# Kernel optimization log

Measured on AMD Instinct MI355X. Metric: run time of the kernel, lower is better.

Reference implementation:

```python
import jax, jax.numpy as jnp
import numpy as np

DOWNSAMPLE = 4
REG = 0.05
SINKHORN_ITERS = 50
LAMBDA_OT = 1.0
LAMBDA_TV = 1.0


def setup_inputs() -> dict:
    key = jax.random.key(0)
    k1, k2 = jax.random.split(key)
    pred = jax.random.uniform(k1, (16, 1, 256, 256), dtype=jnp.float32)
    gt = jax.random.uniform(k2, (16, 1, 256, 256), dtype=jnp.float32)
    return {"pred": pred, "gt": gt, "epoch": 5, "max_epoch": 10}


def _avg_pool(x, k):
    B, C, H, W = x.shape
    return x.reshape(B, C, H // k, k, W // k, k).mean(axis=(3, 5))


def _normalize(x, n):
    # relu then normalize to a distribution; fall back to uniform if sum==0
    x = jnp.maximum(x, 0.0)
    s = x.sum(axis=1, keepdims=True)  # [B,1]
    return jnp.where(s > 0, x / s, jnp.full_like(x, 1.0 / n))


def _curriculum_loss(pred, gt, epoch, max_epoch):
    B = pred.shape[0]
    # --- counting loss: L1 between total counts ---
    pc = pred.reshape(B, -1).sum(axis=1)
    gc = gt.reshape(B, -1).sum(axis=1)
    l_count = jnp.abs(pc - gc).mean()

    t = float(epoch) / float(max(1, max_epoch))
    ot_w = LAMBDA_OT * t
    tv_w = LAMBDA_TV * t

    # --- OT loss (batched Sinkhorn) ---
    pd = _avg_pool(pred, DOWNSAMPLE)
    gd = _avg_pool(gt, DOWNSAMPLE)
    h, w = pd.shape[2], pd.shape[3]
    n = h * w
    ys = jnp.arange(h, dtype=jnp.float32)
    xs = jnp.arange(w, dtype=jnp.float32)
    yy, xx = jnp.meshgrid(ys, xs, indexing="ij")
    yf = yy.reshape(-1)  # [n]
    xf = xx.reshape(-1)
    # squared euclidean cost matrix [n,n], built separably (no [n,n,2] temp)
    M = (yf[:, None] - yf[None, :]) ** 2 + (xf[:, None] - xf[None, :]) ** 2
    K = jnp.exp(-M / REG)  # [n,n]

    a = _normalize(pd.reshape(B, -1), n)  # [B,n]
    b = _normalize(gd.reshape(B, -1), n)

    def step(uv, _):
        u, v = uv
        u = a / (v @ K.T)  # K @ v per sample, batched
        v = b / (u @ K)    # K.T @ u per sample, batched
        return (u, v), None

    ones = jnp.ones((B, n), dtype=pred.dtype)
    (u, v), _ = jax.lax.scan(step, (ones, ones), None, length=SINKHORN_ITERS)
    # cost_b = sum_ij u_i K_ij v_j M_ij
    cost = jnp.einsum("bn,nm,bm->b", u, K * M, v)
    l_ot = cost.mean()

    # --- total variation loss ---
    dx = jnp.abs(pred[:, :, :, 1:] - pred[:, :, :, :-1]).mean()
    dy = jnp.abs(pred[:, :, 1:, :] - pred[:, :, :-1, :]).mean()
    l_tv = dx + dy

    return l_count + ot_w * l_ot + tv_w * l_tv


def reference(pred, gt, epoch, max_epoch):
    return _curriculum_loss(pred, gt, epoch, max_epoch)
```

## Files before the change

kernel.cpp:

```cpp
#include <hip/hip_runtime.h>
#include <math.h>


#define KW1 2.0611536224385578e-09f
#define MW2 8.4967085105831778e-18f
#define RP2 72
#define PDOFF 2048
#define GDOFF 67584

__device__ __forceinline__ float dpp_left(float x) {
  return __int_as_float(__builtin_amdgcn_update_dpp(
      0, __float_as_int(x), 0x111, 0xF, 0xF, true));
}
__device__ __forceinline__ float dpp_right(float x) {
  return __int_as_float(__builtin_amdgcn_update_dpp(
      0, __float_as_int(x), 0x101, 0xF, 0xF, true));
}

__device__ __forceinline__ float ad4(const float4 a, const float4 b) {
  return fabsf(a.x - b.x) + fabsf(a.y - b.y) + fabsf(a.z - b.z) + fabsf(a.w - b.w);
}

__device__ __forceinline__ float agent_ld(const float* p) {
  return __hip_atomic_load(p, __ATOMIC_RELAXED, __HIP_MEMORY_SCOPE_AGENT);
}

__device__ __forceinline__ void hrow4(const float f[4], float h[4]) {
  const float l = dpp_left(f[3]);
  const float r = dpp_right(f[0]);
  h[0] = fmaf(KW1, l + f[1], f[0]);
  h[1] = fmaf(KW1, f[0] + f[2], f[1]);
  h[2] = fmaf(KW1, f[1] + f[3], f[2]);
  h[3] = fmaf(KW1, f[2] + r, f[3]);
}

__device__ __forceinline__ void phase_core(
    const float prev[4][4], float ph[4][4],
    const float cf0[4], const float cf3[4],
    float2 mA, float4 mB, float2 mC, float2 pA, float4 pB, float2 pC,
    float* __restrict__ RT_wr, float* __restrict__ RB_wr, int wb,
    float out0[4], float out3[4]) {
  hrow4(prev[0], ph[0]); hrow4(prev[1], ph[1]);
  hrow4(prev[2], ph[2]); hrow4(prev[3], ph[3]);
  float hm[4], hp[4];
  hm[0] = fmaf(KW1, mA.y + mB.y, mB.x);
  hm[1] = fmaf(KW1, mB.x + mB.z, mB.y);
  hm[2] = fmaf(KW1, mB.y + mB.w, mB.z);
  hm[3] = fmaf(KW1, mB.z + mC.x, mB.w);
  hp[0] = fmaf(KW1, pA.y + pB.y, pB.x);
  hp[1] = fmaf(KW1, pB.x + pB.z, pB.y);
  hp[2] = fmaf(KW1, pB.y + pB.w, pB.z);
  hp[3] = fmaf(KW1, pB.z + pC.x, pB.w);
#pragma unroll
  for (int j = 0; j < 4; ++j)
    out0[j] = cf0[j] * __builtin_amdgcn_rcpf(fmaf(KW1, hm[j] + ph[1][j], ph[0][j]));
#pragma unroll
  for (int j = 0; j < 4; ++j)
    out3[j] = cf3[j] * __builtin_amdgcn_rcpf(fmaf(KW1, ph[2][j] + hp[j], ph[3][j]));
  *(float4*)&RT_wr[wb] = make_float4(out0[0], out0[1], out0[2], out0[3]);
  *(float4*)&RB_wr[wb] = make_float4(out3[0], out3[1], out3[2], out3[3]);
}

__global__ __launch_bounds__(256) void prep_kernel(
    const float* __restrict__ pred, const float* __restrict__ gt,
    float* __restrict__ ws) {
  __shared__ float rbuf[16];
  const int g = blockIdx.x;
  const int im = g >> 4, band = g & 15;
  const int t = threadIdx.x;
  const int ppy = t >> 6, ppx = t & 63;
  const float* pb = pred + im * 65536;
  const float* gb = gt + im * 65536;
  const int sr0 = band * 16 + ppy * 4;
  const int c0 = ppx * 4;

  float4 q[4];
  float ps = 0.f, gs = 0.f, sx = 0.f, sy = 0.f;
#pragma unroll
  for (int r = 0; r < 4; ++r) {
    q[r] = *(const float4*)(pb + (sr0 + r) * 256 + c0);
    const float4 e = *(const float4*)(gb + (sr0 + r) * 256 + c0);
    ps += (q[r].x + q[r].y) + (q[r].z + q[r].w);
    gs += (e.x + e.y) + (e.z + e.w);
    sx += fabsf(q[r].y - q[r].x) + fabsf(q[r].z - q[r].y) + fabsf(q[r].w - q[r].z);
    const float nf = __shfl_down(q[r].x, 1);
    if (ppx < 63) sx += fabsf(nf - q[r].w);
  }
  sy += ad4(q[1], q[0]) + ad4(q[2], q[1]) + ad4(q[3], q[2]);
  if (sr0 + 4 < 256) {
    const float4 qn = *(const float4*)(pb + (sr0 + 4) * 256 + c0);
    sy += ad4(qn, q[3]);
  }
  const int prow = band * 4 + ppy;
  ws[PDOFF + im * 4096 + prow * 64 + ppx] = fmaxf(ps * 0.0625f, 0.f);
  ws[GDOFF + im * 4096 + prow * 64 + ppx] = fmaxf(gs * 0.0625f, 0.f);

  float r0 = ps, r1 = gs, r2 = sx, r3 = sy;
#pragma unroll
  for (int o = 32; o > 0; o >>= 1) {
    r0 += __shfl_down(r0, o); r1 += __shfl_down(r1, o);
    r2 += __shfl_down(r2, o); r3 += __shfl_down(r3, o);
  }
  if ((t & 63) == 0) {
    const int w = t >> 6;
    rbuf[w * 4 + 0] = r0; rbuf[w * 4 + 1] = r1;
    rbuf[w * 4 + 2] = r2; rbuf[w * 4 + 3] = r3;
  }
  __syncthreads();
  if (t == 0) {
    float a0 = 0, a1 = 0, a2 = 0, a3 = 0;
    for (int w = 0; w < 4; ++w) {
      a0 += rbuf[w * 4]; a1 += rbuf[w * 4 + 1];
      a2 += rbuf[w * 4 + 2]; a3 += rbuf[w * 4 + 3];
    }
    ws[g] = a0; ws[256 + g] = a1; ws[512 + g] = a2; ws[768 + g] = a3;
  }
}

__global__ __launch_bounds__(256) void sink_kernel(
    float* __restrict__ ws, const int* __restrict__ epoch,
    const int* __restrict__ max_epoch, float* __restrict__ out,
    unsigned int* __restrict__ cnt) {
  __shared__ float RTu[18 * RP2], RBu[18 * RP2];
  __shared__ float RTv[18 * RP2], RBv[18 * RP2];
  __shared__ float rbuf[24];
  __shared__ int lastflag;

  const int b = blockIdx.x;
  const int t = threadIdx.x;
  const int tyg = t >> 4, tx = t & 15;
  const int y0 = tyg * 4, x0 = tx * 4;

  for (int i = t; i < 18 * RP2; i += 256) {
    RTu[i] = 0.f; RBu[i] = 0.f; RTv[i] = 0.f; RBv[i] = 0.f;
  }

  float pdv[4][4], gdv[4][4];
  float spd = 0.f, sgd = 0.f;
#pragma unroll
  for (int i = 0; i < 4; ++i) {
    const float4 qa = *(const float4*)&ws[PDOFF + b * 4096 + (y0 + i) * 64 + x0];
    pdv[i][0] = qa.x; pdv[i][1] = qa.y; pdv[i][2] = qa.z; pdv[i][3] = qa.w;
    spd += (qa.x + qa.y) + (qa.z + qa.w);
    const float4 qb = *(const float4*)&ws[GDOFF + b * 4096 + (y0 + i) * 64 + x0];
    gdv[i][0] = qb.x; gdv[i][1] = qb.y; gdv[i][2] = qb.z; gdv[i][3] = qb.w;
    sgd += (qb.x + qb.y) + (qb.z + qb.w);
  }
  float r2 = spd, r3 = sgd;
#pragma unroll
  for (int o = 32; o > 0; o >>= 1) { r2 += __shfl_down(r2, o); r3 += __shfl_down(r3, o); }
  if ((t & 63) == 0) { rbuf[(t >> 6) * 2] = r2; rbuf[(t >> 6) * 2 + 1] = r3; }
  __syncthreads();
  if (t == 0) {
    rbuf[16] = rbuf[0] + rbuf[2] + rbuf[4] + rbuf[6];
    rbuf[17] = rbuf[1] + rbuf[3] + rbuf[5] + rbuf[7];
  }
  __syncthreads();
  const float Sp = rbuf[16], Sg = rbuf[17];

  float av[4][4], bv[4][4];
#pragma unroll
  for (int i = 0; i < 4; ++i)
#pragma unroll
    for (int j = 0; j < 4; ++j) {
      av[i][j] = (Sp > 0.f) ? (pdv[i][j] / Sp) : (1.f / 4096.f);
      bv[i][j] = (Sg > 0.f) ? (gdv[i][j] / Sg) : (1.f / 4096.f);
    }

  const int rbb = tyg * RP2 + x0 + 2;
  const int rtb = (tyg + 2) * RP2 + x0 + 2;
  const int wb  = (1 + tyg) * RP2 + 4 + x0;

  float uu[4][4], vv[4][4], uh[4][4], vh[4][4];
#pragma unroll
  for (int i = 0; i < 4; ++i)
#pragma unroll
    for (int j = 0; j < 4; ++j) vv[i][j] = 1.f;
  *(float4*)&RTv[wb] = make_float4(1.f, 1.f, 1.f, 1.f);
  *(float4*)&RBv[wb] = make_float4(1.f, 1.f, 1.f, 1.f);
  __syncthreads();

#pragma unroll 1
  for (int it = 0; it < 50; ++it) {
    {
      const float2 mA = *(const float2*)&RBv[rbb];
      const float4 mB = *(const float4*)&RBv[rbb + 2];
      const float2 mC = *(const float2*)&RBv[rbb + 6];
      const float2 pA = *(const float2*)&RTv[rtb];
      const float4 pB = *(const float4*)&RTv[rtb + 2];
      const float2 pC = *(const float2*)&RTv[rtb + 6];
      if (it != 0) {
#pragma unroll
        for (int j = 0; j < 4; ++j) {
          vv[1][j] = bv[1][j] * __builtin_amdgcn_rcpf(fmaf(KW1, uh[0][j] + uh[2][j], uh[1][j]));
          vv[2][j] = bv[2][j] * __builtin_amdgcn_rcpf(fmaf(KW1, uh[1][j] + uh[3][j], uh[2][j]));
        }
      }
      phase_core(vv, vh, av[0], av[3], mA, mB, mC, pA, pB, pC,
                 RTu, RBu, wb, uu[0], uu[3]);
    }
    __syncthreads();
    {
      const float2 mA = *(const float2*)&RBu[rbb];
      const float4 mB = *(const float4*)&RBu[rbb + 2];
      const float2 mC = *(const float2*)&RBu[rbb + 6];
      const float2 pA = *(const float2*)&RTu[rtb];
      const float4 pB = *(const float4*)&RTu[rtb + 2];
      const float2 pC = *(const float2*)&RTu[rtb + 6];
#pragma unroll
      for (int j = 0; j < 4; ++j) {
        uu[1][j] = av[1][j] * __builtin_amdgcn_rcpf(fmaf(KW1, vh[0][j] + vh[2][j], vh[1][j]));
        uu[2][j] = av[2][j] * __builtin_amdgcn_rcpf(fmaf(KW1, vh[1][j] + vh[3][j], vh[2][j]));
      }
      phase_core(uu, uh, bv[0], bv[3], mA, mB, mC, pA, pB, pC,
                 RTv, RBv, wb, vv[0], vv[3]);
    }
    __syncthreads();
  }
#pragma unroll
  for (int j = 0; j < 4; ++j) {
    vv[1][j] = bv[1][j] * __builtin_amdgcn_rcpf(fmaf(KW1, uh[0][j] + uh[2][j], uh[1][j]));
    vv[2][j] = bv[2][j] * __builtin_amdgcn_rcpf(fmaf(KW1, uh[1][j] + uh[3][j], uh[2][j]));
  }

  float c = 0.f;
  {
    const float2 mA = *(const float2*)&RBv[rbb];
    const float4 mB = *(const float4*)&RBv[rbb + 2];
    const float2 mC = *(const float2*)&RBv[rbb + 6];
    const float2 pA = *(const float2*)&RTv[rtb];
    const float4 pB = *(const float4*)&RTv[rtb + 2];
    const float2 pC = *(const float2*)&RTv[rtb + 6];
    float W[6][6];
    W[0][0] = mA.y; W[0][1] = mB.x; W[0][2] = mB.y;
    W[0][3] = mB.z; W[0][4] = mB.w; W[0][5] = mC.x;
    W[5][0] = pA.y; W[5][1] = pB.x; W[5][2] = pB.y;
    W[5][3] = pB.z; W[5][4] = pB.w; W[5][5] = pC.x;
#pragma unroll
    for (int i = 0; i < 4; ++i) {
      W[1 + i][0] = dpp_left(vv[i][3]);
      W[1 + i][5] = dpp_right(vv[i][0]);
#pragma unroll
      for (int j = 0; j < 4; ++j) W[1 + i][1 + j] = vv[i][j];
    }
#pragma unroll
    for (int i = 0; i < 4; ++i)
#pragma unroll
      for (int j = 0; j < 4; ++j) {
        const float e = (W[i][j + 1] + W[i + 2][j + 1])
                      + (W[i + 1][j] + W[i + 1][j + 2]);
        const float d = (W[i][j] + W[i][j + 2])
                      + (W[i + 2][j] + W[i + 2][j + 2]);
        c += uu[i][j] * fmaf(MW2, d, KW1 * e);
      }
  }
#pragma unroll
  for (int o = 32; o > 0; o >>= 1) c += __shfl_down(c, o);
  if ((t & 63) == 0) rbuf[t >> 6] = c;
  __syncthreads();
  if (t == 0) {
    ws[1024 + b] = rbuf[0] + rbuf[1] + rbuf[2] + rbuf[3];
    __threadfence();
    const unsigned int old = atomicAdd(cnt, 1u);
    lastflag = (old == 15u) ? 1 : 0;
  }
  __syncthreads();

  if (lastflag) {
    __threadfence();
    float myPc = agent_ld(&ws[t]);
    float myGc = agent_ld(&ws[256 + t]);
    float myTx = agent_ld(&ws[512 + t]);
    float myTy = agent_ld(&ws[768 + t]);
#pragma unroll
    for (int o = 8; o > 0; o >>= 1) {
      myPc += __shfl_down(myPc, o, 16);
      myGc += __shfl_down(myGc, o, 16);
    }
    float d = ((t & 15) == 0) ? fabsf(myPc - myGc) : 0.f;
    float ct = (t < 16) ? agent_ld(&ws[1024 + t]) : 0.f;
#pragma unroll
    for (int o = 32; o > 0; o >>= 1) {
      d += __shfl_down(d, o); ct += __shfl_down(ct, o);
      myTx += __shfl_down(myTx, o); myTy += __shfl_down(myTy, o);
    }
    if ((t & 63) == 0) {
      const int w = t >> 6;
      rbuf[w * 4] = d; rbuf[w * 4 + 1] = ct;
      rbuf[w * 4 + 2] = myTx; rbuf[w * 4 + 3] = myTy;
    }
    __syncthreads();
    if (t == 0) {
      float lc = 0, lot = 0, tvx = 0, tvy = 0;
      for (int w = 0; w < 4; ++w) {
        lc += rbuf[w * 4]; lot += rbuf[w * 4 + 1];
        tvx += rbuf[w * 4 + 2]; tvy += rbuf[w * 4 + 3];
      }
      int me = max_epoch[0]; if (me < 1) me = 1;
      const float tt = (float)epoch[0] / (float)me;
      const float ltv = tvx / (16.f * 256.f * 255.f) + tvy / (16.f * 255.f * 256.f);
      out[0] = lc * (1.f / 16.f) + tt * (lot * (1.f / 16.f)) + tt * ltv;
    }
  }
}

__global__ __launch_bounds__(256) void fused_fallback(
    const float* __restrict__ pred, const float* __restrict__ gt,
    float* __restrict__ ws, const int* __restrict__ epoch,
    const int* __restrict__ max_epoch, float* __restrict__ out,
    unsigned int* __restrict__ cnt) {
  __shared__ float RTu[18 * RP2], RBu[18 * RP2];
  __shared__ float RTv[18 * RP2], RBv[18 * RP2];
  __shared__ float rbuf[24];

  const int b = blockIdx.x;
  const int t = threadIdx.x;
  const int tyg = t >> 4, tx = t & 15;
  const int y0 = tyg * 4, x0 = tx * 4;

  for (int i = t; i < 18 * RP2; i += 256) {
    RTu[i] = 0.f; RBu[i] = 0.f; RTv[i] = 0.f; RBv[i] = 0.f;
  }

  const float* pb = pred + b * 65536;
  const float* gb = gt + b * 65536;
  const int sr0 = 4 * y0, sc0 = 4 * x0;

  float pd[4][4], gd[4][4];
  float4 pr0, pr1, pr2, pr3;
  float spraw = 0.f, sgraw = 0.f, sx = 0.f, sy = 0.f;
#pragma unroll
  for (int i = 0; i < 4; ++i) {
    float a0 = 0.f, a1 = 0.f, a2 = 0.f, a3 = 0.f;
    float c0 = 0.f, c1 = 0.f, c2 = 0.f, c3 = 0.f;
#pragma unroll 1
    for (int rr = 0; rr < 4; ++rr) {
      const int r = i * 4 + rr;
      const float* prow = pb + (sr0 + r) * 256 + sc0;
      const float4 q0 = *(const float4*)(prow);
      const float4 q1 = *(const float4*)(prow + 4);
      const float4 q2 = *(const float4*)(prow + 8);
      const float4 q3 = *(const float4*)(prow + 12);
      const float s0 = (q0.x + q0.y) + (q0.z + q0.w);
      const float s1 = (q1.x + q1.y) + (q1.z + q1.w);
      const float s2 = (q2.x + q2.y) + (q2.z + q2.w);
      const float s3 = (q3.x + q3.y) + (q3.z + q3.w);
      a0 += s0; a1 += s1; a2 += s2; a3 += s3;
      spraw += (s0 + s1) + (s2 + s3);
      sx += fabsf(q0.y - q0.x) + fabsf(q0.z - q0.y) + fabsf(q0.w - q0.z)
          + fabsf(q1.x - q0.w)
          + fabsf(q1.y - q1.x) + fabsf(q1.z - q1.y) + fabsf(q1.w - q1.z)
          + fabsf(q2.x - q1.w)
          + fabsf(q2.y - q2.x) + fabsf(q2.z - q2.y) + fabsf(q2.w - q2.z)
          + fabsf(q3.x - q2.w)
          + fabsf(q3.y - q3.x) + fabsf(q3.z - q3.y) + fabsf(q3.w - q3.z);
      const float nf = dpp_right(q0.x);
      if (tx < 15) sx += fabsf(nf - q3.w);
      if (r > 0) sy += ad4(q0, pr0) + ad4(q1, pr1) + ad4(q2, pr2) + ad4(q3, pr3);
      pr0 = q0; pr1 = q1; pr2 = q2; pr3 = q3;
      const float* grow = gb + (sr0 + r) * 256 + sc0;
      const float4 g0 = *(const float4*)(grow);
      const float4 g1 = *(const float4*)(grow + 4);
      const float4 g2 = *(const float4*)(grow + 8);
      const float4 g3 = *(const float4*)(grow + 12);
      const float u0 = (g0.x + g0.y) + (g0.z + g0.w);
      const float u1 = (g1.x + g1.y) + (g1.z + g1.w);
      const float u2 = (g2.x + g2.y) + (g2.z + g2.w);
      const float u3 = (g3.x + g3.y) + (g3.z + g3.w);
      c0 += u0; c1 += u1; c2 += u2; c3 += u3;
      sgraw += (u0 + u1) + (u2 + u3);
    }
    pd[i][0] = a0; pd[i][1] = a1; pd[i][2] = a2; pd[i][3] = a3;
    gd[i][0] = c0; gd[i][1] = c1; gd[i][2] = c2; gd[i][3] = c3;
  }
  if (tyg < 15) {
    const float* prow = pb + (sr0 + 16) * 256 + sc0;
    sy += ad4(*(const float4*)(prow), pr0) + ad4(*(const float4*)(prow + 4), pr1)
        + ad4(*(const float4*)(prow + 8), pr2) + ad4(*(const float4*)(prow + 12), pr3);
  }

  float spd = 0.f, sgd = 0.f;
#pragma unroll
  for (int i = 0; i < 4; ++i)
#pragma unroll
    for (int j = 0; j < 4; ++j) {
      pd[i][j] = fmaxf(pd[i][j] * 0.0625f, 0.f); spd += pd[i][j];
      gd[i][j] = fmaxf(gd[i][j] * 0.0625f, 0.f); sgd += gd[i][j];
    }

  float r0 = spraw, r1 = sgraw, r2 = spd, r3 = sgd, r4 = sx, r5 = sy;
#pragma unroll
  for (int o = 32; o > 0; o >>= 1) {
    r0 += __shfl_down(r0, o); r1 += __shfl_down(r1, o);
    r2 += __shfl_down(r2, o); r3 += __shfl_down(r3, o);
    r4 += __shfl_down(r4, o); r5 += __shfl_down(r5, o);
  }
  if ((t & 63) == 0) {
    const int w = t >> 6;
    rbuf[w * 6 + 0] = r0; rbuf[w * 6 + 1] = r1; rbuf[w * 6 + 2] = r2;
    rbuf[w * 6 + 3] = r3; rbuf[w * 6 + 4] = r4; rbuf[w * 6 + 5] = r5;
  }
  __syncthreads();
  if (t == 0) {
    float a0 = 0, a1 = 0, a2 = 0, a3 = 0, a4 = 0, a5 = 0;
    for (int w = 0; w < 4; ++w) {
      a0 += rbuf[w * 6 + 0]; a1 += rbuf[w * 6 + 1]; a2 += rbuf[w * 6 + 2];
      a3 += rbuf[w * 6 + 3]; a4 += rbuf[w * 6 + 4]; a5 += rbuf[w * 6 + 5];
    }
    ws[b] = a0; ws[16 + b] = a1; ws[48 + b] = a4; ws[64 + b] = a5;
    rbuf[0] = a2; rbuf[1] = a3;
  }
  __syncthreads();
  const float Sp = rbuf[0], Sg = rbuf[1];

  float av[4][4], bv[4][4];
#pragma unroll
  for (int i = 0; i < 4; ++i)
#pragma unroll
    for (int j = 0; j < 4; ++j) {
      av[i][j] = (Sp > 0.f) ? (pd[i][j] / Sp) : (1.f / 4096.f);
      bv[i][j] = (Sg > 0.f) ? (gd[i][j] / Sg) : (1.f / 4096.f);
    }

  const int rbb = tyg * RP2 + x0 + 2;
  const int rtb = (tyg + 2) * RP2 + x0 + 2;
  const int wb  = (1 + tyg) * RP2 + 4 + x0;

  float uu[4][4], vv[4][4], uh[4][4], vh[4][4];
#pragma unroll
  for (int i = 0; i < 4; ++i)
#pragma unroll
    for (int j = 0; j < 4; ++j) vv[i][j] = 1.f;
  *(float4*)&RTv[wb] = make_float4(1.f, 1.f, 1.f, 1.f);
  *(float4*)&RBv[wb] = make_float4(1.f, 1.f, 1.f, 1.f);
  __syncthreads();

#pragma unroll 1
  for (int it = 0; it < 50; ++it) {
    {
      const float2 mA = *(const float2*)&RBv[rbb];
      const float4 mB = *(const float4*)&RBv[rbb + 2];
      const float2 mC = *(const float2*)&RBv[rbb + 6];
      const float2 pA = *(const float2*)&RTv[rtb];
      const float4 pB = *(const float4*)&RTv[rtb + 2];
      const float2 pC = *(const float2*)&RTv[rtb + 6];
      if (it != 0) {
#pragma unroll
        for (int j = 0; j < 4; ++j) {
          vv[1][j] = bv[1][j] * __builtin_amdgcn_rcpf(fmaf(KW1, uh[0][j] + uh[2][j], uh[1][j]));
          vv[2][j] = bv[2][j] * __builtin_amdgcn_rcpf(fmaf(KW1, uh[1][j] + uh[3][j], uh[2][j]));
        }
      }
      phase_core(vv, vh, av[0], av[3], mA, mB, mC, pA, pB, pC,
                 RTu, RBu, wb, uu[0], uu[3]);
    }
    __syncthreads();
    {
      const float2 mA = *(const float2*)&RBu[rbb];
      const float4 mB = *(const float4*)&RBu[rbb + 2];
      const float2 mC = *(const float2*)&RBu[rbb + 6];
      const float2 pA = *(const float2*)&RTu[rtb];
      const float4 pB = *(const float4*)&RTu[rtb + 2];
      const float2 pC = *(const float2*)&RTu[rtb + 6];
#pragma unroll
      for (int j = 0; j < 4; ++j) {
        uu[1][j] = av[1][j] * __builtin_amdgcn_rcpf(fmaf(KW1, vh[0][j] + vh[2][j], vh[1][j]));
        uu[2][j] = av[2][j] * __builtin_amdgcn_rcpf(fmaf(KW1, vh[1][j] + vh[3][j], vh[2][j]));
      }
      phase_core(uu, uh, bv[0], bv[3], mA, mB, mC, pA, pB, pC,
                 RTv, RBv, wb, vv[0], vv[3]);
    }
    __syncthreads();
  }
#pragma unroll
  for (int j = 0; j < 4; ++j) {
    vv[1][j] = bv[1][j] * __builtin_amdgcn_rcpf(fmaf(KW1, uh[0][j] + uh[2][j], uh[1][j]));
    vv[2][j] = bv[2][j] * __builtin_amdgcn_rcpf(fmaf(KW1, uh[1][j] + uh[3][j], uh[2][j]));
  }

  float c = 0.f;
  {
    const float2 mA = *(const float2*)&RBv[rbb];
    const float4 mB = *(const float4*)&RBv[rbb + 2];
    const float2 mC = *(const float2*)&RBv[rbb + 6];
    const float2 pA = *(const float2*)&RTv[rtb];
    const float4 pB = *(const float4*)&RTv[rtb + 2];
    const float2 pC = *(const float2*)&RTv[rtb + 6];
    float W[6][6];
    W[0][0] = mA.y; W[0][1] = mB.x; W[0][2] = mB.y;
    W[0][3] = mB.z; W[0][4] = mB.w; W[0][5] = mC.x;
    W[5][0] = pA.y; W[5][1] = pB.x; W[5][2] = pB.y;
    W[5][3] = pB.z; W[5][4] = pB.w; W[5][5] = pC.x;
#pragma unroll
    for (int i = 0; i < 4; ++i) {
      W[1 + i][0] = dpp_left(vv[i][3]);
      W[1 + i][5] = dpp_right(vv[i][0]);
#pragma unroll
      for (int j = 0; j < 4; ++j) W[1 + i][1 + j] = vv[i][j];
    }
#pragma unroll
    for (int i = 0; i < 4; ++i)
#pragma unroll
      for (int j = 0; j < 4; ++j) {
        const float e = (W[i][j + 1] + W[i + 2][j + 1])
                      + (W[i + 1][j] + W[i + 1][j + 2]);
        const float d = (W[i][j] + W[i][j + 2])
                      + (W[i + 2][j] + W[i + 2][j + 2]);
        c += uu[i][j] * fmaf(MW2, d, KW1 * e);
      }
  }
#pragma unroll
  for (int o = 32; o > 0; o >>= 1) c += __shfl_down(c, o);
  if ((t & 63) == 0) rbuf[t >> 6] = c;
  __syncthreads();
  if (t == 0) {
    ws[32 + b] = rbuf[0] + rbuf[1] + rbuf[2] + rbuf[3];
    __threadfence();
    const unsigned int old = atomicAdd(cnt, 1u);
    if (old == 15u) {
      __threadfence();
      float lc = 0.f, lot = 0.f, tvx = 0.f, tvy = 0.f;
      for (int k = 0; k < 16; ++k) {
        const float p = agent_ld(&ws[k]);
        const float g = agent_ld(&ws[16 + k]);
        const float ct = agent_ld(&ws[32 + k]);
        const float x = agent_ld(&ws[48 + k]);
        const float y = agent_ld(&ws[64 + k]);
        lc += fabsf(p - g); lot += ct; tvx += x; tvy += y;
      }
      int me = max_epoch[0]; if (me < 1) me = 1;
      const float tt = (float)epoch[0] / (float)me;
      const float ltv = tvx / (16.f * 256.f * 255.f) + tvy / (16.f * 255.f * 256.f);
      out[0] = lc * (1.f / 16.f) + tt * (lot * (1.f / 16.f)) + tt * ltv;
    }
  }
}

extern "C" void kernel_launch(void* const* d_in, const int* in_sizes, int n_in,
                              void* d_out, int out_size, void* d_ws, size_t ws_size,
                              hipStream_t stream) {
  const float* pred = (const float*)d_in[0];
  const float* gt   = (const float*)d_in[1];
  const int* epoch  = (const int*)d_in[2];
  const int* max_ep = (const int*)d_in[3];
  float* out = (float*)d_out;
  float* ws  = (float*)d_ws;

  if (ws_size >= 600000) {
    unsigned int* cnt = (unsigned int*)((char*)d_ws + 4160);
    hipMemsetAsync(cnt, 0, 4, stream);
    prep_kernel<<<dim3(256), dim3(256), 0, stream>>>(pred, gt, ws);
    sink_kernel<<<dim3(16), dim3(256), 0, stream>>>(ws, epoch, max_ep, out, cnt);
  } else {
    unsigned int* cnt = (unsigned int*)((char*)d_ws + 384);
    hipMemsetAsync(cnt, 0, 4, stream);
    fused_fallback<<<dim3(16), dim3(256), 0, stream>>>(pred, gt, ws, epoch,
                                                       max_ep, out, cnt);
  }
}
```

Measured before the change: 111.5 us.

## Remap Sinkhorn grid so each lane owns a 16-column row strip

The sink kernel now gives each lane one grid row and 16 columns (a warp covers 64 rows of a 16-column strip), instead of 4x4 tiles per thread. Vertical neighbors come from wavefront row-shift DPP moves within the wave, so only the two strip-edge columns go through shared memory each half-iteration. This cuts LDS traffic and the halo loads and stores per iteration. In exchange, every element now needs two cross-lane DPP ops per half step. Lanes 0 and 63 rely on the DPP bound-control zero fill to supply the zero grid boundary.

```diff
diff --git a/kernel.cpp b/kernel.cpp
--- a/kernel.cpp
+++ b/kernel.cpp
@@ -8,23 +8,247 @@
 #define PDOFF 2048
 #define GDOFF 67584
 
+__device__ __forceinline__ float dpp_right(float x) {
+  return __int_as_float(__builtin_amdgcn_update_dpp(
+      0, __float_as_int(x), 0x101, 0xF, 0xF, true));
+}
 __device__ __forceinline__ float dpp_left(float x) {
   return __int_as_float(__builtin_amdgcn_update_dpp(
       0, __float_as_int(x), 0x111, 0xF, 0xF, true));
 }
-__device__ __forceinline__ float dpp_right(float x) {
+__device__ __forceinline__ float wshr1(float x) {
   return __int_as_float(__builtin_amdgcn_update_dpp(
-      0, __float_as_int(x), 0x101, 0xF, 0xF, true));
+      0, __float_as_int(x), 0x138, 0xF, 0xF, true));
+}
+__device__ __forceinline__ float wshl1(float x) {
+  return __int_as_float(__builtin_amdgcn_update_dpp(
+      0, __float_as_int(x), 0x130, 0xF, 0xF, true));
 }
 
 __device__ __forceinline__ float ad4(const float4 a, const float4 b) {
   return fabsf(a.x - b.x) + fabsf(a.y - b.y) + fabsf(a.z - b.z) + fabsf(a.w - b.w);
 }
-
 __device__ __forceinline__ float agent_ld(const float* p) {
   return __hip_atomic_load(p, __ATOMIC_RELAXED, __HIP_MEMORY_SCOPE_AGENT);
 }
 
+__global__ __launch_bounds__(256) void prep_kernel(
+    const float* __restrict__ pred, const float* __restrict__ gt,
+    float* __restrict__ ws) {
+  __shared__ float rbuf[16];
+  const int g = blockIdx.x;
+  const int im = g >> 4, band = g & 15;
+  const int t = threadIdx.x;
+  const int ppy = t >> 6, ppx = t & 63;
+  const float* pb = pred + im * 65536;
+  const float* gb = gt + im * 65536;
+  const int sr0 = band * 16 + ppy * 4;
+  const int c0 = ppx * 4;
+
+  float4 q[4];
+  float ps = 0.f, gs = 0.f, sx = 0.f, sy = 0.f;
+#pragma unroll
+  for (int r = 0; r < 4; ++r) {
+    q[r] = *(const float4*)(pb + (sr0 + r) * 256 + c0);
+    const float4 e = *(const float4*)(gb + (sr0 + r) * 256 + c0);
+    ps += (q[r].x + q[r].y) + (q[r].z + q[r].w);
+    gs += (e.x + e.y) + (e.z + e.w);
+    sx += fabsf(q[r].y - q[r].x) + fabsf(q[r].z - q[r].y) + fabsf(q[r].w - q[r].z);
+    const float nf = __shfl_down(q[r].x, 1);
+    if (ppx < 63) sx += fabsf(nf - q[r].w);
+  }
+  sy += ad4(q[1], q[0]) + ad4(q[2], q[1]) + ad4(q[3], q[2]);
+  if (sr0 + 4 < 256) {
+    const float4 qn = *(const float4*)(pb + (sr0 + 4) * 256 + c0);
+    sy += ad4(qn, q[3]);
+  }
+  const int prow = band * 4 + ppy;
+  ws[PDOFF + im * 4096 + prow * 64 + ppx] = fmaxf(ps * 0.0625f, 0.f);
+  ws[GDOFF + im * 4096 + prow * 64 + ppx] = fmaxf(gs * 0.0625f, 0.f);
+
+  float r0 = ps, r1 = gs, r2 = sx, r3 = sy;
+#pragma unroll
+  for (int o = 32; o > 0; o >>= 1) {
+    r0 += __shfl_down(r0, o); r1 += __shfl_down(r1, o);
+    r2 += __shfl_down(r2, o); r3 += __shfl_down(r3, o);
+  }
+  if ((t & 63) == 0) {
+    const int w = t >> 6;
+    rbuf[w * 4 + 0] = r0; rbuf[w * 4 + 1] = r1;
+    rbuf[w * 4 + 2] = r2; rbuf[w * 4 + 3] = r3;
+  }
+  __syncthreads();
+  if (t == 0) {
+    float a0 = 0, a1 = 0, a2 = 0, a3 = 0;
+    for (int w = 0; w < 4; ++w) {
+      a0 += rbuf[w * 4]; a1 += rbuf[w * 4 + 1];
+      a2 += rbuf[w * 4 + 2]; a3 += rbuf[w * 4 + 3];
+    }
+    ws[g] = a0; ws[256 + g] = a1; ws[512 + g] = a2; ws[768 + g] = a3;
+  }
+}
+
+__global__ __launch_bounds__(256) void sink_kernel(
+    float* __restrict__ ws, const int* __restrict__ epoch,
+    const int* __restrict__ max_epoch, float* __restrict__ out,
+    unsigned int* __restrict__ cnt) {
+  __shared__ float SuL[6 * 64], SuR[6 * 64], SvL[6 * 64], SvR[6 * 64];
+  __shared__ float rbuf[24];
+  __shared__ int lastflag;
+
+  const int b = blockIdx.x;
+  const int t = threadIdx.x;
+  const int w = t >> 6;
+  const int l = t & 63;
+
+  for (int i = t; i < 6 * 64; i += 256) {
+    SuL[i] = 0.f; SuR[i] = 0.f; SvL[i] = 0.f; SvR[i] = 0.f;
+  }
+  __syncthreads();
+  SvL[(w + 1) * 64 + l] = 1.f;
+  SvR[(w + 1) * 64 + l] = 1.f;
+
+  float av[16], bv[16];
+  {
+    const float* P = &ws[PDOFF + b * 4096 + l * 64 + w * 16];
+    const float* G = &ws[GDOFF + b * 4096 + l * 64 + w * 16];
+    float spd = 0.f, sgd = 0.f;
+#pragma unroll
+    for (int c4 = 0; c4 < 4; ++c4) {
+      const float4 qa = *(const float4*)(P + 4 * c4);
+      av[4 * c4] = qa.x; av[4 * c4 + 1] = qa.y;
+      av[4 * c4 + 2] = qa.z; av[4 * c4 + 3] = qa.w;
+      spd += (qa.x + qa.y) + (qa.z + qa.w);
+      const float4 qb = *(const float4*)(G + 4 * c4);
+      bv[4 * c4] = qb.x; bv[4 * c4 + 1] = qb.y;
+      bv[4 * c4 + 2] = qb.z; bv[4 * c4 + 3] = qb.w;
+      sgd += (qb.x + qb.y) + (qb.z + qb.w);
+    }
+#pragma unroll
+    for (int o = 32; o > 0; o >>= 1) {
+      spd += __shfl_down(spd, o); sgd += __shfl_down(sgd, o);
+    }
+    if (l == 0) { rbuf[w * 2] = spd; rbuf[w * 2 + 1] = sgd; }
+  }
+  __syncthreads();
+  const float Sp = rbuf[0] + rbuf[2] + rbuf[4] + rbuf[6];
+  const float Sg = rbuf[1] + rbuf[3] + rbuf[5] + rbuf[7];
+#pragma unroll
+  for (int c = 0; c < 16; ++c) {
+    av[c] = (Sp > 0.f) ? (av[c] / Sp) : (1.f / 4096.f);
+    bv[c] = (Sg > 0.f) ? (bv[c] / Sg) : (1.f / 4096.f);
+  }
+
+  const int rdL = w * 64 + l;
+  const int rdR = (w + 2) * 64 + l;
+  const int wr  = (w + 1) * 64 + l;
+
+  float uu[16], vv[16], hh[16];
+#pragma unroll
+  for (int c = 0; c < 16; ++c) vv[c] = 1.f;
+  __syncthreads();
+
+#pragma unroll 1
+  for (int it = 0; it < 50; ++it) {
+    {
+      const float xl = SvR[rdL];
+      const float xr = SvL[rdR];
+      hh[0] = fmaf(KW1, xl + vv[1], vv[0]);
+#pragma unroll
+      for (int c = 1; c < 15; ++c) hh[c] = fmaf(KW1, vv[c - 1] + vv[c + 1], vv[c]);
+      hh[15] = fmaf(KW1, vv[14] + xr, vv[15]);
+#pragma unroll
+      for (int c = 0; c < 16; ++c) {
+        const float up = wshr1(hh[c]);
+        const float dn = wshl1(hh[c]);
+        uu[c] = av[c] * __builtin_amdgcn_rcpf(fmaf(KW1, up + dn, hh[c]));
+      }
+      SuL[wr] = uu[0]; SuR[wr] = uu[15];
+    }
+    __syncthreads();
+    {
+      const float xl = SuR[rdL];
+      const float xr = SuL[rdR];
+      hh[0] = fmaf(KW1, xl + uu[1], uu[0]);
+#pragma unroll
+      for (int c = 1; c < 15; ++c) hh[c] = fmaf(KW1, uu[c - 1] + uu[c + 1], uu[c]);
+      hh[15] = fmaf(KW1, uu[14] + xr, uu[15]);
+#pragma unroll
+      for (int c = 0; c < 16; ++c) {
+        const float up = wshr1(hh[c]);
+        const float dn = wshl1(hh[c]);
+        vv[c] = bv[c] * __builtin_amdgcn_rcpf(fmaf(KW1, up + dn, hh[c]));
+      }
+      SvL[wr] = vv[0]; SvR[wr] = vv[15];
+    }
+    __syncthreads();
+  }
+
+  float c = 0.f;
+  {
+    const float xl = SvR[rdL];
+    const float xr = SvL[rdR];
+#pragma unroll
+    for (int cc = 0; cc < 16; ++cc) {
+      const float vl = (cc == 0) ? xl : vv[cc - 1];
+      const float vr = (cc == 15) ? xr : vv[cc + 1];
+      const float s = vl + vr;
+      const float e = (wshr1(vv[cc]) + wshl1(vv[cc])) + s;
+      const float d = wshr1(s) + wshl1(s);
+      c += uu[cc] * fmaf(MW2, d, KW1 * e);
+    }
+  }
+#pragma unroll
+  for (int o = 32; o > 0; o >>= 1) c += __shfl_down(c, o);
+  if (l == 0) rbuf[8 + w] = c;
+  __syncthreads();
+  if (t == 0) {
+    ws[1024 + b] = rbuf[8] + rbuf[9] + rbuf[10] + rbuf[11];
+    __threadfence();
+    const unsigned int old = atomicAdd(cnt, 1u);
+    lastflag = (old == 15u) ? 1 : 0;
+  }
+  __syncthreads();
+
+  if (lastflag) {
+    __threadfence();
+    float myPc = agent_ld(&ws[t]);
+    float myGc = agent_ld(&ws[256 + t]);
+    float myTx = agent_ld(&ws[512 + t]);
+    float myTy = agent_ld(&ws[768 + t]);
+#pragma unroll
+    for (int o = 8; o > 0; o >>= 1) {
+      myPc += __shfl_down(myPc, o, 16);
+      myGc += __shfl_down(myGc, o, 16);
+    }
+    float d = ((t & 15) == 0) ? fabsf(myPc - myGc) : 0.f;
+    float ct = (t < 16) ? agent_ld(&ws[1024 + t]) : 0.f;
+#pragma unroll
+    for (int o = 32; o > 0; o >>= 1) {
+      d += __shfl_down(d, o); ct += __shfl_down(ct, o);
+      myTx += __shfl_down(myTx, o); myTy += __shfl_down(myTy, o);
+    }
+    if ((t & 63) == 0) {
+      const int ww = t >> 6;
+      rbuf[ww * 4] = d; rbuf[ww * 4 + 1] = ct;
+      rbuf[ww * 4 + 2] = myTx; rbuf[ww * 4 + 3] = myTy;
+    }
+    __syncthreads();
+    if (t == 0) {
+      float lc = 0, lot = 0, tvx = 0, tvy = 0;
+      for (int ww = 0; ww < 4; ++ww) {
+        lc += rbuf[ww * 4]; lot += rbuf[ww * 4 + 1];
+        tvx += rbuf[ww * 4 + 2]; tvy += rbuf[ww * 4 + 3];
+      }
+      int me = max_epoch[0]; if (me < 1) me = 1;
+      const float tt = (float)epoch[0] / (float)me;
+      const float ltv = tvx / (16.f * 256.f * 255.f) + tvy / (16.f * 255.f * 256.f);
+      out[0] = lc * (1.f / 16.f) + tt * (lot * (1.f / 16.f)) + tt * ltv;
+    }
+  }
+}
+
+#define SPW1 2.0611536224385578e-09f
 __device__ __forceinline__ void hrow4(const float f[4], float h[4]) {
   const float l = dpp_left(f[3]);
   const float r = dpp_right(f[0]);
@@ -33,7 +257,6 @@
   h[2] = fmaf(KW1, f[1] + f[3], f[2]);
   h[3] = fmaf(KW1, f[2] + r, f[3]);
 }
-
 __device__ __forceinline__ void phase_core(
     const float prev[4][4], float ph[4][4],
     const float cf0[4], const float cf3[4],
@@ -59,249 +282,6 @@
     out3[j] = cf3[j] * __builtin_amdgcn_rcpf(fmaf(KW1, ph[2][j] + hp[j], ph[3][j]));
   *(float4*)&RT_wr[wb] = make_float4(out0[0], out0[1], out0[2], out0[3]);
   *(float4*)&RB_wr[wb] = make_float4(out3[0], out3[1], out3[2], out3[3]);
-}
-
-__global__ __launch_bounds__(256) void prep_kernel(
-    const float* __restrict__ pred, const float* __restrict__ gt,
-    float* __restrict__ ws) {
-  __shared__ float rbuf[16];
-  const int g = blockIdx.x;
-  const int im = g >> 4, band = g & 15;
-  const int t = threadIdx.x;
-  const int ppy = t >> 6, ppx = t & 63;
-  const float* pb = pred + im * 65536;
-  const float* gb = gt + im * 65536;
-  const int sr0 = band * 16 + ppy * 4;
-  const int c0 = ppx * 4;
-
-  float4 q[4];
-  float ps = 0.f, gs = 0.f, sx = 0.f, sy = 0.f;
-#pragma unroll
-  for (int r = 0; r < 4; ++r) {
-    q[r] = *(const float4*)(pb + (sr0 + r) * 256 + c0);
-    const float4 e = *(const float4*)(gb + (sr0 + r) * 256 + c0);
-    ps += (q[r].x + q[r].y) + (q[r].z + q[r].w);
-    gs += (e.x + e.y) + (e.z + e.w);
-    sx += fabsf(q[r].y - q[r].x) + fabsf(q[r].z - q[r].y) + fabsf(q[r].w - q[r].z);
-    const float nf = __shfl_down(q[r].x, 1);
-    if (ppx < 63) sx += fabsf(nf - q[r].w);
-  }
-  sy += ad4(q[1], q[0]) + ad4(q[2], q[1]) + ad4(q[3], q[2]);
-  if (sr0 + 4 < 256) {
-    const float4 qn = *(const float4*)(pb + (sr0 + 4) * 256 + c0);
-    sy += ad4(qn, q[3]);
-  }
-  const int prow = band * 4 + ppy;
-  ws[PDOFF + im * 4096 + prow * 64 + ppx] = fmaxf(ps * 0.0625f, 0.f);
-  ws[GDOFF + im * 4096 + prow * 64 + ppx] = fmaxf(gs * 0.0625f, 0.f);
-
-  float r0 = ps, r1 = gs, r2 = sx, r3 = sy;
-#pragma unroll
-  for (int o = 32; o > 0; o >>= 1) {
-    r0 += __shfl_down(r0, o); r1 += __shfl_down(r1, o);
-    r2 += __shfl_down(r2, o); r3 += __shfl_down(r3, o);
-  }
-  if ((t & 63) == 0) {
-    const int w = t >> 6;
-    rbuf[w * 4 + 0] = r0; rbuf[w * 4 + 1] = r1;
-    rbuf[w * 4 + 2] = r2; rbuf[w * 4 + 3] = r3;
-  }
-  __syncthreads();
-  if (t == 0) {
-    float a0 = 0, a1 = 0, a2 = 0, a3 = 0;
-    for (int w = 0; w < 4; ++w) {
-      a0 += rbuf[w * 4]; a1 += rbuf[w * 4 + 1];
-      a2 += rbuf[w * 4 + 2]; a3 += rbuf[w * 4 + 3];
-    }
-    ws[g] = a0; ws[256 + g] = a1; ws[512 + g] = a2; ws[768 + g] = a3;
-  }
-}
-
-__global__ __launch_bounds__(256) void sink_kernel(
-    float* __restrict__ ws, const int* __restrict__ epoch,
-    const int* __restrict__ max_epoch, float* __restrict__ out,
-    unsigned int* __restrict__ cnt) {
-  __shared__ float RTu[18 * RP2], RBu[18 * RP2];
-  __shared__ float RTv[18 * RP2], RBv[18 * RP2];
-  __shared__ float rbuf[24];
-  __shared__ int lastflag;
-
-  const int b = blockIdx.x;
-  const int t = threadIdx.x;
-  const int tyg = t >> 4, tx = t & 15;
-  const int y0 = tyg * 4, x0 = tx * 4;
-
-  for (int i = t; i < 18 * RP2; i += 256) {
-    RTu[i] = 0.f; RBu[i] = 0.f; RTv[i] = 0.f; RBv[i] = 0.f;
-  }
-
-  float pdv[4][4], gdv[4][4];
-  float spd = 0.f, sgd = 0.f;
-#pragma unroll
-  for (int i = 0; i < 4; ++i) {
-    const float4 qa = *(const float4*)&ws[PDOFF + b * 4096 + (y0 + i) * 64 + x0];
-    pdv[i][0] = qa.x; pdv[i][1] = qa.y; pdv[i][2] = qa.z; pdv[i][3] = qa.w;
-    spd += (qa.x + qa.y) + (qa.z + qa.w);
-    const float4 qb = *(const float4*)&ws[GDOFF + b * 4096 + (y0 + i) * 64 + x0];
-    gdv[i][0] = qb.x; gdv[i][1] = qb.y; gdv[i][2] = qb.z; gdv[i][3] = qb.w;
-    sgd += (qb.x + qb.y) + (qb.z + qb.w);
-  }
-  float r2 = spd, r3 = sgd;
-#pragma unroll
-  for (int o = 32; o > 0; o >>= 1) { r2 += __shfl_down(r2, o); r3 += __shfl_down(r3, o); }
-  if ((t & 63) == 0) { rbuf[(t >> 6) * 2] = r2; rbuf[(t >> 6) * 2 + 1] = r3; }
-  __syncthreads();
-  if (t == 0) {
-    rbuf[16] = rbuf[0] + rbuf[2] + rbuf[4] + rbuf[6];
-    rbuf[17] = rbuf[1] + rbuf[3] + rbuf[5] + rbuf[7];
-  }
-  __syncthreads();
-  const float Sp = rbuf[16], Sg = rbuf[17];
-
-  float av[4][4], bv[4][4];
-#pragma unroll
-  for (int i = 0; i < 4; ++i)
-#pragma unroll
-    for (int j = 0; j < 4; ++j) {
-      av[i][j] = (Sp > 0.f) ? (pdv[i][j] / Sp) : (1.f / 4096.f);
-      bv[i][j] = (Sg > 0.f) ? (gdv[i][j] / Sg) : (1.f / 4096.f);
-    }
-
-  const int rbb = tyg * RP2 + x0 + 2;
-  const int rtb = (tyg + 2) * RP2 + x0 + 2;
-  const int wb  = (1 + tyg) * RP2 + 4 + x0;
-
-  float uu[4][4], vv[4][4], uh[4][4], vh[4][4];
-#pragma unroll
-  for (int i = 0; i < 4; ++i)
-#pragma unroll
-    for (int j = 0; j < 4; ++j) vv[i][j] = 1.f;
-  *(float4*)&RTv[wb] = make_float4(1.f, 1.f, 1.f, 1.f);
-  *(float4*)&RBv[wb] = make_float4(1.f, 1.f, 1.f, 1.f);
-  __syncthreads();
-
-#pragma unroll 1
-  for (int it = 0; it < 50; ++it) {
-    {
-      const float2 mA = *(const float2*)&RBv[rbb];
-      const float4 mB = *(const float4*)&RBv[rbb + 2];
-      const float2 mC = *(const float2*)&RBv[rbb + 6];
-      const float2 pA = *(const float2*)&RTv[rtb];
-      const float4 pB = *(const float4*)&RTv[rtb + 2];
-      const float2 pC = *(const float2*)&RTv[rtb + 6];
-      if (it != 0) {
-#pragma unroll
-        for (int j = 0; j < 4; ++j) {
-          vv[1][j] = bv[1][j] * __builtin_amdgcn_rcpf(fmaf(KW1, uh[0][j] + uh[2][j], uh[1][j]));
-          vv[2][j] = bv[2][j] * __builtin_amdgcn_rcpf(fmaf(KW1, uh[1][j] + uh[3][j], uh[2][j]));
-        }
-      }
-      phase_core(vv, vh, av[0], av[3], mA, mB, mC, pA, pB, pC,
-                 RTu, RBu, wb, uu[0], uu[3]);
-    }
-    __syncthreads();
-    {
-      const float2 mA = *(const float2*)&RBu[rbb];
-      const float4 mB = *(const float4*)&RBu[rbb + 2];
-      const float2 mC = *(const float2*)&RBu[rbb + 6];
-      const float2 pA = *(const float2*)&RTu[rtb];
-      const float4 pB = *(const float4*)&RTu[rtb + 2];
-      const float2 pC = *(const float2*)&RTu[rtb + 6];
-#pragma unroll
-      for (int j = 0; j < 4; ++j) {
-        uu[1][j] = av[1][j] * __builtin_amdgcn_rcpf(fmaf(KW1, vh[0][j] + vh[2][j], vh[1][j]));
-        uu[2][j] = av[2][j] * __builtin_amdgcn_rcpf(fmaf(KW1, vh[1][j] + vh[3][j], vh[2][j]));
-      }
-      phase_core(uu, uh, bv[0], bv[3], mA, mB, mC, pA, pB, pC,
-                 RTv, RBv, wb, vv[0], vv[3]);
-    }
-    __syncthreads();
-  }
-#pragma unroll
-  for (int j = 0; j < 4; ++j) {
-    vv[1][j] = bv[1][j] * __builtin_amdgcn_rcpf(fmaf(KW1, uh[0][j] + uh[2][j], uh[1][j]));
-    vv[2][j] = bv[2][j] * __builtin_amdgcn_rcpf(fmaf(KW1, uh[1][j] + uh[3][j], uh[2][j]));
-  }
-
-  float c = 0.f;
-  {
-    const float2 mA = *(const float2*)&RBv[rbb];
-    const float4 mB = *(const float4*)&RBv[rbb + 2];
-    const float2 mC = *(const float2*)&RBv[rbb + 6];
-    const float2 pA = *(const float2*)&RTv[rtb];
-    const float4 pB = *(const float4*)&RTv[rtb + 2];
-    const float2 pC = *(const float2*)&RTv[rtb + 6];
-    float W[6][6];
-    W[0][0] = mA.y; W[0][1] = mB.x; W[0][2] = mB.y;
-    W[0][3] = mB.z; W[0][4] = mB.w; W[0][5] = mC.x;
-    W[5][0] = pA.y; W[5][1] = pB.x; W[5][2] = pB.y;
-    W[5][3] = pB.z; W[5][4] = pB.w; W[5][5] = pC.x;
-#pragma unroll
-    for (int i = 0; i < 4; ++i) {
-      W[1 + i][0] = dpp_left(vv[i][3]);
-      W[1 + i][5] = dpp_right(vv[i][0]);
-#pragma unroll
-      for (int j = 0; j < 4; ++j) W[1 + i][1 + j] = vv[i][j];
-    }
-#pragma unroll
-    for (int i = 0; i < 4; ++i)
-#pragma unroll
-      for (int j = 0; j < 4; ++j) {
-        const float e = (W[i][j + 1] + W[i + 2][j + 1])
-                      + (W[i + 1][j] + W[i + 1][j + 2]);
-        const float d = (W[i][j] + W[i][j + 2])
-                      + (W[i + 2][j] + W[i + 2][j + 2]);
-        c += uu[i][j] * fmaf(MW2, d, KW1 * e);
-      }
-  }
-#pragma unroll
-  for (int o = 32; o > 0; o >>= 1) c += __shfl_down(c, o);
-  if ((t & 63) == 0) rbuf[t >> 6] = c;
-  __syncthreads();
-  if (t == 0) {
-    ws[1024 + b] = rbuf[0] + rbuf[1] + rbuf[2] + rbuf[3];
-    __threadfence();
-    const unsigned int old = atomicAdd(cnt, 1u);
-    lastflag = (old == 15u) ? 1 : 0;
-  }
-  __syncthreads();
-
-  if (lastflag) {
-    __threadfence();
-    float myPc = agent_ld(&ws[t]);
-    float myGc = agent_ld(&ws[256 + t]);
-    float myTx = agent_ld(&ws[512 + t]);
-    float myTy = agent_ld(&ws[768 + t]);
-#pragma unroll
-    for (int o = 8; o > 0; o >>= 1) {
-      myPc += __shfl_down(myPc, o, 16);
-      myGc += __shfl_down(myGc, o, 16);
-    }
-    float d = ((t & 15) == 0) ? fabsf(myPc - myGc) : 0.f;
-    float ct = (t < 16) ? agent_ld(&ws[1024 + t]) : 0.f;
-#pragma unroll
-    for (int o = 32; o > 0; o >>= 1) {
-      d += __shfl_down(d, o); ct += __shfl_down(ct, o);
-      myTx += __shfl_down(myTx, o); myTy += __shfl_down(myTy, o);
-    }
-    if ((t & 63) == 0) {
-      const int w = t >> 6;
-      rbuf[w * 4] = d; rbuf[w * 4 + 1] = ct;
-      rbuf[w * 4 + 2] = myTx; rbuf[w * 4 + 3] = myTy;
-    }
-    __syncthreads();
-    if (t == 0) {
-      float lc = 0, lot = 0, tvx = 0, tvy = 0;
-      for (int w = 0; w < 4; ++w) {
-        lc += rbuf[w * 4]; lot += rbuf[w * 4 + 1];
-        tvx += rbuf[w * 4 + 2]; tvy += rbuf[w * 4 + 3];
-      }
-      int me = max_epoch[0]; if (me < 1) me = 1;
-      const float tt = (float)epoch[0] / (float)me;
-      const float ltv = tvx / (16.f * 256.f * 255.f) + tvy / (16.f * 255.f * 256.f);
-      out[0] = lc * (1.f / 16.f) + tt * (lot * (1.f / 16.f)) + tt * ltv;
-    }
-  }
 }
 
 __global__ __launch_bounds__(256) void fused_fallback(
```

Measured after the change: 103.9 us. 6.8% less time.
